# Kernel tuning notes

Measured on AMD Instinct MI355X. Metric: run time of the kernel, lower is better.

Reference implementation:

```python
import jax, jax.numpy as jnp
import numpy as np

N_NODES = 50000
N_EDGES = 800000
NODE_DIM = 8
EDGE_DIM = 4
ENC = 64
ROUNDS = 3
OUT_DIM = 5
NEG_SLOPE = 0.2


def _segment_softmax(s, dst, n):
    # per-destination-neighborhood softmax over edge scores s: [E]
    smax = jax.ops.segment_max(s, dst, num_segments=n)
    ex = jnp.exp(s - smax[dst])
    denom = jax.ops.segment_sum(ex, dst, num_segments=n)
    return ex / denom[dst]


def _gatv2(h, e_enc, src, dst, Wl, Wr, We, att, b):
    # GATv2Conv, heads=1, share_weights=False, no dropout (eval)
    xl = h @ Wl            # [N, ENC] source transform
    xr = h @ Wr            # [N, ENC] dest transform
    ep = e_enc @ We        # [E, ENC] edge transform
    m = xl[src] + xr[dst] + ep               # [E, ENC]
    s = jax.nn.leaky_relu(m, NEG_SLOPE) @ att  # [E]
    alpha = _segment_softmax(s, dst, h.shape[0])
    out = jax.ops.segment_sum(alpha[:, None] * xl[src], dst, num_segments=h.shape[0])
    return out + b


def _gnn_stack(h, e_enc, src, dst, Wl, Wr, We, att, b):
    for r in range(ROUNDS):
        h = _gatv2(h, e_enc, src, dst, Wl[r], Wr[r], We[r], att[r], b[r])
        if r < ROUNDS - 1:
            h = jax.nn.relu(h)
    return h


def setup_inputs() -> dict:
    key = jax.random.key(0)
    ks = jax.random.split(key, 24)
    f32 = jnp.float32
    p = lambda k, shp: 0.1 * jax.random.normal(k, shp, dtype=f32)
    return {
        "x": jax.random.normal(ks[0], (N_NODES, NODE_DIM), dtype=f32),
        "edge_attr": jax.random.normal(ks[1], (N_EDGES, EDGE_DIM), dtype=f32),
        "W_node": p(ks[2], (NODE_DIM, ENC)), "b_node": jnp.zeros((ENC,), f32),
        "W_edge": p(ks[3], (EDGE_DIM, ENC)), "b_edge": jnp.zeros((ENC,), f32),
        "actor_Wl": p(ks[4], (ROUNDS, ENC, ENC)),
        "actor_Wr": p(ks[5], (ROUNDS, ENC, ENC)),
        "actor_We": p(ks[6], (ROUNDS, ENC, ENC)),
        "actor_att": p(ks[7], (ROUNDS, ENC)),
        "actor_b": jnp.zeros((ROUNDS, ENC), f32),
        "critic_Wl": p(ks[8], (ROUNDS, ENC, ENC)),
        "critic_Wr": p(ks[9], (ROUNDS, ENC, ENC)),
        "critic_We": p(ks[10], (ROUNDS, ENC, ENC)),
        "critic_att": p(ks[11], (ROUNDS, ENC)),
        "critic_b": jnp.zeros((ROUNDS, ENC), f32),
        "W_act": p(ks[12], (ENC, OUT_DIM)), "b_act": jnp.zeros((OUT_DIM,), f32),
        "W_val": p(ks[13], (ENC, 1)), "b_val": jnp.zeros((1,), f32),
        "src": jax.random.randint(ks[14], (N_EDGES,), 0, N_NODES, dtype=jnp.int32),
        "dst": jax.random.randint(ks[15], (N_EDGES,), 0, N_NODES, dtype=jnp.int32),
    }


def reference(x, edge_attr, W_node, b_node, W_edge, b_edge,
              actor_Wl, actor_Wr, actor_We, actor_att, actor_b,
              critic_Wl, critic_Wr, critic_We, critic_att, critic_b,
              W_act, b_act, W_val, b_val, src, dst):
    h0 = x @ W_node + b_node          # node encoder (single SlimFC, no activation)
    e0 = edge_attr @ W_edge + b_edge  # edge encoder
    ha = _gnn_stack(h0, e0, src, dst, actor_Wl, actor_Wr, actor_We, actor_att, actor_b)
    hc = _gnn_stack(h0, e0, src, dst, critic_Wl, critic_Wr, critic_We, critic_att, critic_b)
    actions = jnp.tanh(ha @ W_act + b_act)  # action decoder, tanh activation
    values = hc @ W_val + b_val             # value decoder, no activation
    return jnp.concatenate([actions, values], axis=-1)  # [N, OUT_DIM+1]
```

## Files before the change

kernel.cpp:

```cpp
#include <hip/hip_runtime.h>
#include <math.h>

#define N_NODES 50000
#define N_EDGES 800000
#define ENC 64
#define ROUNDS 3
#define NEG_SLOPE 0.2f

typedef unsigned int u32;

__device__ __forceinline__ float lrelu(float m) {
  return m > 0.f ? m : NEG_SLOPE * m;
}

__global__ void k_hist(const int* __restrict__ dst, int* __restrict__ deg) {
  int i = blockIdx.x * blockDim.x + threadIdx.x;
  int stride = gridDim.x * blockDim.x;
  for (; i < N_EDGES; i += stride) atomicAdd(&deg[dst[i]], 1);
}

#define SCAN_BLOCKS ((N_NODES + 255) / 256)

__global__ void __launch_bounds__(256) k_red(const int* __restrict__ deg,
                                             int* __restrict__ part) {
  __shared__ int sm[256];
  int bi = blockIdx.x, t = threadIdx.x;
  int i = bi * 256 + t;
  sm[t] = (i < N_NODES) ? deg[i] : 0;
  __syncthreads();
  for (int off = 128; off > 0; off >>= 1) {
    if (t < off) sm[t] += sm[t + off];
    __syncthreads();
  }
  if (t == 0) part[bi] = sm[0];
}

__global__ void __launch_bounds__(256) k_scanp(int* __restrict__ part) {
  __shared__ int sm[256];
  int t = threadIdx.x;
  int v = (t < SCAN_BLOCKS) ? part[t] : 0;
  sm[t] = v;
  __syncthreads();
  for (int off = 1; off < 256; off <<= 1) {
    int u = (t >= off) ? sm[t - off] : 0;
    __syncthreads();
    sm[t] += u;
    __syncthreads();
  }
  if (t < SCAN_BLOCKS) part[t] = sm[t] - v;
}

__global__ void __launch_bounds__(256) k_csr(int* __restrict__ degcur,
                                             const int* __restrict__ part,
                                             int* __restrict__ row_start) {
  __shared__ int sm[256];
  int bi = blockIdx.x, t = threadIdx.x;
  int i = bi * 256 + t;
  int v = (i < N_NODES) ? degcur[i] : 0;
  sm[t] = v;
  __syncthreads();
  for (int off = 1; off < 256; off <<= 1) {
    int u = (t >= off) ? sm[t - off] : 0;
    __syncthreads();
    sm[t] += u;
    __syncthreads();
  }
  int excl = sm[t] - v + part[bi];
  if (i < N_NODES) {
    row_start[i] = excl;
    degcur[i] = excl;
    if (i == N_NODES - 1) row_start[N_NODES] = excl + v;
  }
}

__global__ void k_scatter(const int* __restrict__ src, const int* __restrict__ dst,
                          const float* __restrict__ ea, int* __restrict__ cursor,
                          int* __restrict__ srcs, float* __restrict__ ea_perm) {
  int i = blockIdx.x * blockDim.x + threadIdx.x;
  int stride = gridDim.x * blockDim.x;
  for (; i < N_EDGES; i += stride) {
    int d = dst[i];
    int pos = atomicAdd(&cursor[d], 1);
    srcs[pos] = src[i];
    ((float4*)ea_perm)[pos] = ((const float4*)ea)[i];
  }
}

__global__ void k_encode(const float* __restrict__ x, const float* __restrict__ Wn,
                         const float* __restrict__ bn, float* __restrict__ h0,
                         const float* __restrict__ W_edge, const float* __restrict__ b_edge,
                         const float* __restrict__ aWe, const float* __restrict__ cWe,
                         float* __restrict__ wcomb, float* __restrict__ bcomb) {
  __shared__ float lw[8 * ENC];
  __shared__ float lb[ENC];
  int t = threadIdx.x;
  if (blockIdx.x == 0) {
    int i = t >> 6, d = t & 63;
    for (int sr = 0; sr < 6; ++sr) {
      const float* We = (sr < 3) ? (aWe + sr * ENC * ENC) : (cWe + (sr - 3) * ENC * ENC);
      float sum = 0.f;
      for (int k = 0; k < ENC; ++k) sum += W_edge[i * ENC + k] * We[k * ENC + d];
      wcomb[sr * 4 * ENC + i * ENC + d] = sum;
      if (t < ENC) {
        float bs = 0.f;
        for (int k = 0; k < ENC; ++k) bs += b_edge[k] * We[k * ENC + t];
        bcomb[sr * ENC + t] = bs;
      }
    }
  }
  for (int i = t; i < 8 * ENC; i += blockDim.x) lw[i] = Wn[i];
  if (t < ENC) lb[t] = bn[t];
  __syncthreads();
  int wid = t >> 6, lane = t & 63;
  int nwaves = (blockDim.x >> 6) * gridDim.x;
  int w = blockIdx.x * (blockDim.x >> 6) + wid;
  for (int n = w; n < N_NODES; n += nwaves) {
    const float4* xr4 = (const float4*)(x + n * 8);
    float4 a = xr4[0], b = xr4[1];
    float acc = lb[lane];
    acc += a.x * lw[0 * ENC + lane] + a.y * lw[1 * ENC + lane] +
           a.z * lw[2 * ENC + lane] + a.w * lw[3 * ENC + lane];
    acc += b.x * lw[4 * ENC + lane] + b.y * lw[5 * ENC + lane] +
           b.z * lw[6 * ENC + lane] + b.w * lw[7 * ENC + lane];
    h0[n * ENC + lane] = acc;
  }
}

__global__ void __launch_bounds__(256) k_gemm2(const float* __restrict__ hinA,
                                               const float* __restrict__ hinC,
                                               const float* __restrict__ WlA,
                                               const float* __restrict__ WrA,
                                               const float* __restrict__ bcA,
                                               float* __restrict__ xlA_,
                                               float* __restrict__ xrA_,
                                               const float* __restrict__ WlC,
                                               const float* __restrict__ WrC,
                                               const float* __restrict__ bcC,
                                               float* __restrict__ xlC_,
                                               float* __restrict__ xrC_) {
  const int stk = blockIdx.y;
  const float* hin = stk ? hinC : hinA;
  const float* Wl = stk ? WlC : WlA;
  const float* Wr = stk ? WrC : WrA;
  const float* bc = stk ? bcC : bcA;
  float* xl = stk ? xlC_ : xlA_;
  float* xr = stk ? xrC_ : xrA_;
  __shared__ float lw[2 * ENC * ENC];
  __shared__ float lh[64 * ENC];
  int t = threadIdx.x;
  {
    const float4* wl4 = (const float4*)Wl;
    const float4* wr4 = (const float4*)Wr;
    float4* lw4 = (float4*)lw;
#pragma unroll
    for (int i = 0; i < 4; ++i) lw4[t + 256 * i] = wl4[t + 256 * i];
#pragma unroll
    for (int i = 0; i < 4; ++i) lw4[1024 + t + 256 * i] = wr4[t + 256 * i];
  }
  int base = blockIdx.x * 64;
  {
    const float4* h4 = (const float4*)hin;
    float4* lh4 = (float4*)lh;
    int maxi = N_NODES * 16 - 1;
#pragma unroll
    for (int i = 0; i < 4; ++i) {
      int idx = t + 256 * i;
      int gi = base * 16 + idx;
      if (gi > maxi) gi = maxi;
      lh4[idx] = h4[gi];
    }
  }
  __syncthreads();
  int wid = t >> 6, lane = t & 63;
  int msel = lane >> 5, cc = lane & 31;
  const float2* lw2 = (const float2*)lw;
  float* outp = msel ? xr : xl;
  float2 bcv = make_float2(0.f, 0.f);
  if (msel) bcv = ((const float2*)bc)[cc];
#pragma unroll
  for (int chunk = 0; chunk < 4; ++chunk) {
    int n0 = wid * 16 + chunk * 4;
    float a00 = 0.f, a01 = 0.f, a10 = 0.f, a11 = 0.f;
    float a20 = 0.f, a21 = 0.f, a30 = 0.f, a31 = 0.f;
    const float4* r0 = (const float4*)(lh + (n0 + 0) * ENC);
    const float4* r1 = (const float4*)(lh + (n0 + 1) * ENC);
    const float4* r2 = (const float4*)(lh + (n0 + 2) * ENC);
    const float4* r3 = (const float4*)(lh + (n0 + 3) * ENC);
#pragma unroll
    for (int k4 = 0; k4 < 16; ++k4) {
      float4 h0 = r0[k4], h1 = r1[k4], h2 = r2[k4], h3 = r3[k4];
      float2 w0 = lw2[msel * 2048 + (k4 * 4 + 0) * 32 + cc];
      float2 w1 = lw2[msel * 2048 + (k4 * 4 + 1) * 32 + cc];
      float2 w2 = lw2[msel * 2048 + (k4 * 4 + 2) * 32 + cc];
      float2 w3 = lw2[msel * 2048 + (k4 * 4 + 3) * 32 + cc];
      a00 += h0.x * w0.x + h0.y * w1.x + h0.z * w2.x + h0.w * w3.x;
      a01 += h0.x * w0.y + h0.y * w1.y + h0.z * w2.y + h0.w * w3.y;
      a10 += h1.x * w0.x + h1.y * w1.x + h1.z * w2.x + h1.w * w3.x;
      a11 += h1.x * w0.y + h1.y * w1.y + h1.z * w2.y + h1.w * w3.y;
      a20 += h2.x * w0.x + h2.y * w1.x + h2.z * w2.x + h2.w * w3.x;
      a21 += h2.x * w0.y + h2.y * w1.y + h2.z * w2.y + h2.w * w3.y;
      a30 += h3.x * w0.x + h3.y * w1.x + h3.z * w2.x + h3.w * w3.x;
      a31 += h3.x * w0.y + h3.y * w1.y + h3.z * w2.y + h3.w * w3.y;
    }
    int ng = base + n0;
    if (ng + 0 < N_NODES) *(float2*)(outp + (size_t)(ng + 0) * ENC + cc * 2) = make_float2(a00 + bcv.x, a01 + bcv.y);
    if (ng + 1 < N_NODES) *(float2*)(outp + (size_t)(ng + 1) * ENC + cc * 2) = make_float2(a10 + bcv.x, a11 + bcv.y);
    if (ng + 2 < N_NODES) *(float2*)(outp + (size_t)(ng + 2) * ENC + cc * 2) = make_float2(a20 + bcv.x, a21 + bcv.y);
    if (ng + 3 < N_NODES) *(float2*)(outp + (size_t)(ng + 3) * ENC + cc * 2) = make_float2(a30 + bcv.x, a31 + bcv.y);
  }
}

template <int RELU>
__global__ void __launch_bounds__(256) k_attn(
    const int* __restrict__ row_start, const int* __restrict__ srcs,
    const float* __restrict__ ea_perm,
    const float* __restrict__ xla, const float* __restrict__ xra,
    const float* __restrict__ xlc, const float* __restrict__ xrc,
    const float* __restrict__ wca, const float* __restrict__ wcc,
    const float* __restrict__ atta, const float* __restrict__ attc,
    const float* __restrict__ Ba, const float* __restrict__ Bc,
    float* __restrict__ ha, float* __restrict__ hc) {
  const float NEG_INF = __int_as_float(0xff800000u);
  const int stk = blockIdx.y;
  const float* xl = stk ? xlc : xla;
  const float* xr = stk ? xrc : xra;
  const float* wc = stk ? wcc : wca;
  const float* att = stk ? attc : atta;
  const float* B = stk ? Bc : Ba;
  float* hout = stk ? hc : ha;
  int t = threadIdx.x;
  int wid = t >> 6, lane = t & 63;
  int g = lane >> 4;
  int l16 = lane & 15;
  float4 w0 = ((const float4*)(wc + 0 * ENC))[l16];
  float4 w1 = ((const float4*)(wc + 1 * ENC))[l16];
  float4 w2 = ((const float4*)(wc + 2 * ENC))[l16];
  float4 w3 = ((const float4*)(wc + 3 * ENC))[l16];
  float4 at = ((const float4*)att)[l16];
  float4 bv = ((const float4*)B)[l16];
  int nw = (blockDim.x >> 6) * gridDim.x;
  for (int n = blockIdx.x * (blockDim.x >> 6) + wid; n < N_NODES; n += nw) {
    int rs = row_start[n], re = row_start[n + 1];
    float4 outv;
    if (re > rs) {
      float4 xrn = ((const float4*)(xr + (size_t)n * ENC))[l16];
      float m = -1e30f, den = 0.f;
      float4 acc = make_float4(0.f, 0.f, 0.f, 0.f);
      int cnt0 = re - rs; if (cnt0 > 16) cnt0 = 16;
      float eav = (lane < 4 * cnt0) ? ea_perm[(size_t)rs * 4 + lane] : 0.f;
      int sval = (lane < cnt0) ? srcs[rs + lane] : 0;
      for (int base = rs; base < re; base += 16) {
        int cnt = re - base; if (cnt > 16) cnt = 16;
        float eav_c = eav;
        int sval_c = sval;
        int nb = base + 16;
        if (nb < re) {
          int cn = re - nb; if (cn > 16) cn = 16;
          eav = (lane < 4 * cn) ? ea_perm[(size_t)nb * 4 + lane] : 0.f;
          sval = (lane < cn) ? srcs[nb + lane] : 0;
        }
        float4 la[4];
        bool act[4];
#pragma unroll
        for (int j = 0; j < 4; ++j) {
          int jj = j * 4 + g;
          act[j] = jj < cnt;
          int sj = __shfl(sval_c, act[j] ? jj : (cnt - 1));
          la[j] = ((const float4*)xl)[sj * 16 + l16];
        }
        float px[4];
#pragma unroll
        for (int j = 0; j < 4; ++j) {
          int jj = j * 4 + g;
          float av0 = __shfl(eav_c, jj * 4 + 0);
          float av1 = __shfl(eav_c, jj * 4 + 1);
          float av2 = __shfl(eav_c, jj * 4 + 2);
          float av3 = __shfl(eav_c, jj * 4 + 3);
          float p = lrelu(la[j].x + xrn.x + av0 * w0.x + av1 * w1.x + av2 * w2.x + av3 * w3.x) * at.x;
          p += lrelu(la[j].y + xrn.y + av0 * w0.y + av1 * w1.y + av2 * w2.y + av3 * w3.y) * at.y;
          p += lrelu(la[j].z + xrn.z + av0 * w0.z + av1 * w1.z + av2 * w2.z + av3 * w3.z) * at.z;
          p += lrelu(la[j].w + xrn.w + av0 * w0.w + av1 * w1.w + av2 * w2.w + av3 * w3.w) * at.w;
          p += __shfl_xor(p, 1);
          p += __shfl_xor(p, 2);
          p += __shfl_xor(p, 4);
          p += __shfl_xor(p, 8);
          px[j] = act[j] ? p : NEG_INF;
        }
#pragma unroll
        for (int j = 0; j < 4; ++j) {
          float mn = fmaxf(m, px[j]);
          float sc = __expf(m - mn);
          float ex = __expf(px[j] - mn);
          den = den * sc + ex;
          acc.x = acc.x * sc + ex * la[j].x;
          acc.y = acc.y * sc + ex * la[j].y;
          acc.z = acc.z * sc + ex * la[j].z;
          acc.w = acc.w * sc + ex * la[j].w;
          m = mn;
        }
      }
#pragma unroll
      for (int d = 16; d <= 32; d <<= 1) {
        float m2 = __shfl_xor(m, d);
        float dn2 = __shfl_xor(den, d);
        float a2x = __shfl_xor(acc.x, d), a2y = __shfl_xor(acc.y, d);
        float a2z = __shfl_xor(acc.z, d), a2w = __shfl_xor(acc.w, d);
        float mn = fmaxf(m, m2);
        float s1 = __expf(m - mn), s2 = __expf(m2 - mn);
        den = den * s1 + dn2 * s2;
        acc.x = acc.x * s1 + a2x * s2;
        acc.y = acc.y * s1 + a2y * s2;
        acc.z = acc.z * s1 + a2z * s2;
        acc.w = acc.w * s1 + a2w * s2;
        m = mn;
      }
      float inv = 1.f / den;
      outv = make_float4(acc.x * inv + bv.x, acc.y * inv + bv.y,
                         acc.z * inv + bv.z, acc.w * inv + bv.w);
    } else {
      outv = bv;
    }
    if (RELU) {
      outv.x = fmaxf(outv.x, 0.f);
      outv.y = fmaxf(outv.y, 0.f);
      outv.z = fmaxf(outv.z, 0.f);
      outv.w = fmaxf(outv.w, 0.f);
    }
    if (g == 0) ((float4*)(hout + (size_t)n * ENC))[l16] = outv;
  }
}

__global__ void k_dec(const float* __restrict__ ha, const float* __restrict__ hc,
                      const float* __restrict__ Wa, const float* __restrict__ ba,
                      const float* __restrict__ Wv, const float* __restrict__ bv,
                      float* __restrict__ out) {
  int t = threadIdx.x;
  int wid = t >> 6, lane = t & 63;
  int nw = (blockDim.x >> 6) * gridDim.x;
  int w = blockIdx.x * (blockDim.x >> 6) + wid;
  for (int n = w; n < N_NODES; n += nw) {
    float hva = ha[(size_t)n * ENC + lane];
    float hvc = hc[(size_t)n * ENC + lane];
#pragma unroll
    for (int j = 0; j < 5; ++j) {
      float p = hva * Wa[lane * 5 + j];
      p += __shfl_xor(p, 1);
      p += __shfl_xor(p, 2);
      p += __shfl_xor(p, 4);
      p += __shfl_xor(p, 8);
      p += __shfl_xor(p, 16);
      p += __shfl_xor(p, 32);
      if (lane == 0) out[n * 6 + j] = tanhf(p + ba[j]);
    }
    float p = hvc * Wv[lane];
    p += __shfl_xor(p, 1);
    p += __shfl_xor(p, 2);
    p += __shfl_xor(p, 4);
    p += __shfl_xor(p, 8);
    p += __shfl_xor(p, 16);
    p += __shfl_xor(p, 32);
    if (lane == 0) out[n * 6 + 5] = p + bv[0];
  }
}

extern "C" void kernel_launch(void* const* d_in, const int* in_sizes, int n_in,
                              void* d_out, int out_size, void* d_ws, size_t ws_size,
                              hipStream_t stream) {
  const float* x    = (const float*)d_in[0];
  const float* ea   = (const float*)d_in[1];
  const float* Wn   = (const float*)d_in[2];
  const float* bn   = (const float*)d_in[3];
  const float* Wedg = (const float*)d_in[4];
  const float* bedg = (const float*)d_in[5];
  const float* aWl  = (const float*)d_in[6];
  const float* aWr  = (const float*)d_in[7];
  const float* aWe  = (const float*)d_in[8];
  const float* aAtt = (const float*)d_in[9];
  const float* aB   = (const float*)d_in[10];
  const float* cWl  = (const float*)d_in[11];
  const float* cWr  = (const float*)d_in[12];
  const float* cWe  = (const float*)d_in[13];
  const float* cAtt = (const float*)d_in[14];
  const float* cB   = (const float*)d_in[15];
  const float* Wa   = (const float*)d_in[16];
  const float* ba   = (const float*)d_in[17];
  const float* Wv   = (const float*)d_in[18];
  const float* bv   = (const float*)d_in[19];
  const int* src    = (const int*)d_in[20];
  const int* dst    = (const int*)d_in[21];
  float* out = (float*)d_out;

  char* w = (char*)d_ws;
  size_t off = 0;
  auto alloc = [&](size_t bytes) -> char* {
    char* p = w + off;
    off = (off + bytes + 255) & ~(size_t)255;
    return p;
  };
  float* h0  = (float*)alloc((size_t)N_NODES * ENC * 4);
  float* hA  = (float*)alloc((size_t)N_NODES * ENC * 4);
  float* hC  = (float*)alloc((size_t)N_NODES * ENC * 4);
  float* xlA = (float*)alloc((size_t)N_NODES * ENC * 4);
  float* xrA = (float*)alloc((size_t)N_NODES * ENC * 4);
  float* xlC = (float*)alloc((size_t)N_NODES * ENC * 4);
  float* xrC = (float*)alloc((size_t)N_NODES * ENC * 4);
  int* srcs      = (int*)alloc((size_t)N_EDGES * 4);
  float* ea_perm = (float*)alloc((size_t)N_EDGES * 16);
  int* row_start = (int*)alloc((size_t)(N_NODES + 1) * 4);
  int* cursor    = (int*)alloc((size_t)N_NODES * 4);
  int* part      = (int*)alloc(256 * 4);
  float* wcomb   = (float*)alloc(6 * 4 * ENC * 4);
  float* bcomb   = (float*)alloc(6 * ENC * 4);

  hipMemsetAsync(cursor, 0, (size_t)N_NODES * 4, stream);
  k_hist<<<2048, 256, 0, stream>>>(dst, cursor);
  k_red<<<SCAN_BLOCKS, 256, 0, stream>>>(cursor, part);
  k_scanp<<<1, 256, 0, stream>>>(part);
  k_csr<<<SCAN_BLOCKS, 256, 0, stream>>>(cursor, part, row_start);
  k_scatter<<<2048, 256, 0, stream>>>(src, dst, ea, cursor, srcs, ea_perm);

  k_encode<<<512, 256, 0, stream>>>(x, Wn, bn, h0, Wedg, bedg, aWe, cWe, wcomb, bcomb);

  const int GEMM_TILES = (N_NODES + 63) / 64;

  for (int r = 0; r < ROUNDS; ++r) {
    const float* hinA = (r == 0) ? h0 : hA;
    const float* hinC = (r == 0) ? h0 : hC;
    k_gemm2<<<dim3(GEMM_TILES, 2), 256, 0, stream>>>(
        hinA, hinC, aWl + r * ENC * ENC, aWr + r * ENC * ENC, bcomb + r * ENC, xlA, xrA,
        cWl + r * ENC * ENC, cWr + r * ENC * ENC, bcomb + (3 + r) * ENC, xlC, xrC);
    if (r < ROUNDS - 1)
      k_attn<1><<<dim3(2048, 2), 256, 0, stream>>>(row_start, srcs, ea_perm, xlA, xrA, xlC, xrC,
                                                   wcomb + r * 4 * ENC, wcomb + (3 + r) * 4 * ENC,
                                                   aAtt + r * ENC, cAtt + r * ENC,
                                                   aB + r * ENC, cB + r * ENC, hA, hC);
    else
      k_attn<0><<<dim3(2048, 2), 256, 0, stream>>>(row_start, srcs, ea_perm, xlA, xrA, xlC, xrC,
                                                   wcomb + r * 4 * ENC, wcomb + (3 + r) * 4 * ENC,
                                                   aAtt + r * ENC, cAtt + r * ENC,
                                                   aB + r * ENC, cB + r * ENC, hA, hC);
  }
  k_dec<<<1024, 256, 0, stream>>>(hA, hC, Wa, ba, Wv, bv, out);
}
```

Baseline: 845.6 us.

## Interleave actor/critic xl/xr rows and process both stacks in one attention wave

The GEMM now writes actor and critic projections into combined arrays of 128 floats per node. The attention kernel handles both stacks in a single pass: each half-wave of 16 lanes serves one stack, and each 512-byte row gather fetches both stacks' features for an edge. This halves the number of passes over the CSR edge lists, source indices and edge attributes, and doubles the bytes per gathered row, so random-access efficiency should improve. In exchange, each wave now covers two edges per step instead of four, and the launch grid is halved, so per-node latency may rise.

Measured after the change: 689.8 us. 1.23x faster.

```diff
diff --git a/kernel.cpp b/kernel.cpp
--- a/kernel.cpp
+++ b/kernel.cpp
@@ -131,20 +131,16 @@
                                                const float* __restrict__ WlA,
                                                const float* __restrict__ WrA,
                                                const float* __restrict__ bcA,
-                                               float* __restrict__ xlA_,
-                                               float* __restrict__ xrA_,
                                                const float* __restrict__ WlC,
                                                const float* __restrict__ WrC,
                                                const float* __restrict__ bcC,
-                                               float* __restrict__ xlC_,
-                                               float* __restrict__ xrC_) {
+                                               float* __restrict__ xl_comb,
+                                               float* __restrict__ xr_comb) {
   const int stk = blockIdx.y;
   const float* hin = stk ? hinC : hinA;
   const float* Wl = stk ? WlC : WlA;
   const float* Wr = stk ? WrC : WrA;
   const float* bc = stk ? bcC : bcA;
-  float* xl = stk ? xlC_ : xlA_;
-  float* xr = stk ? xrC_ : xrA_;
   __shared__ float lw[2 * ENC * ENC];
   __shared__ float lh[64 * ENC];
   int t = threadIdx.x;
@@ -174,7 +170,7 @@
   int wid = t >> 6, lane = t & 63;
   int msel = lane >> 5, cc = lane & 31;
   const float2* lw2 = (const float2*)lw;
-  float* outp = msel ? xr : xl;
+  float* outp = (msel ? xr_comb : xl_comb) + stk * 64;
   float2 bcv = make_float2(0.f, 0.f);
   if (msel) bcv = ((const float2*)bc)[cc];
 #pragma unroll
@@ -203,10 +199,10 @@
       a31 += h3.x * w0.y + h3.y * w1.y + h3.z * w2.y + h3.w * w3.y;
     }
     int ng = base + n0;
-    if (ng + 0 < N_NODES) *(float2*)(outp + (size_t)(ng + 0) * ENC + cc * 2) = make_float2(a00 + bcv.x, a01 + bcv.y);
-    if (ng + 1 < N_NODES) *(float2*)(outp + (size_t)(ng + 1) * ENC + cc * 2) = make_float2(a10 + bcv.x, a11 + bcv.y);
-    if (ng + 2 < N_NODES) *(float2*)(outp + (size_t)(ng + 2) * ENC + cc * 2) = make_float2(a20 + bcv.x, a21 + bcv.y);
-    if (ng + 3 < N_NODES) *(float2*)(outp + (size_t)(ng + 3) * ENC + cc * 2) = make_float2(a30 + bcv.x, a31 + bcv.y);
+    if (ng + 0 < N_NODES) *(float2*)(outp + (size_t)(ng + 0) * 128 + cc * 2) = make_float2(a00 + bcv.x, a01 + bcv.y);
+    if (ng + 1 < N_NODES) *(float2*)(outp + (size_t)(ng + 1) * 128 + cc * 2) = make_float2(a10 + bcv.x, a11 + bcv.y);
+    if (ng + 2 < N_NODES) *(float2*)(outp + (size_t)(ng + 2) * 128 + cc * 2) = make_float2(a20 + bcv.x, a21 + bcv.y);
+    if (ng + 3 < N_NODES) *(float2*)(outp + (size_t)(ng + 3) * 128 + cc * 2) = make_float2(a30 + bcv.x, a31 + bcv.y);
   }
 }
 
@@ -214,36 +210,34 @@
 __global__ void __launch_bounds__(256) k_attn(
     const int* __restrict__ row_start, const int* __restrict__ srcs,
     const float* __restrict__ ea_perm,
-    const float* __restrict__ xla, const float* __restrict__ xra,
-    const float* __restrict__ xlc, const float* __restrict__ xrc,
+    const float* __restrict__ xl_comb, const float* __restrict__ xr_comb,
     const float* __restrict__ wca, const float* __restrict__ wcc,
     const float* __restrict__ atta, const float* __restrict__ attc,
     const float* __restrict__ Ba, const float* __restrict__ Bc,
     float* __restrict__ ha, float* __restrict__ hc) {
   const float NEG_INF = __int_as_float(0xff800000u);
-  const int stk = blockIdx.y;
-  const float* xl = stk ? xlc : xla;
-  const float* xr = stk ? xrc : xra;
-  const float* wc = stk ? wcc : wca;
-  const float* att = stk ? attc : atta;
-  const float* B = stk ? Bc : Ba;
-  float* hout = stk ? hc : ha;
   int t = threadIdx.x;
   int wid = t >> 6, lane = t & 63;
-  int g = lane >> 4;
+  int g2 = lane >> 5;
+  int sl = (lane >> 4) & 1;
   int l16 = lane & 15;
-  float4 w0 = ((const float4*)(wc + 0 * ENC))[l16];
-  float4 w1 = ((const float4*)(wc + 1 * ENC))[l16];
-  float4 w2 = ((const float4*)(wc + 2 * ENC))[l16];
-  float4 w3 = ((const float4*)(wc + 3 * ENC))[l16];
-  float4 at = ((const float4*)att)[l16];
-  float4 bv = ((const float4*)B)[l16];
+  int q32 = lane & 31;
+  const float* wcS = sl ? wcc : wca;
+  const float* attS = sl ? attc : atta;
+  const float* BS = sl ? Bc : Ba;
+  float* houtS = sl ? hc : ha;
+  float4 w0 = ((const float4*)(wcS + 0 * ENC))[l16];
+  float4 w1 = ((const float4*)(wcS + 1 * ENC))[l16];
+  float4 w2 = ((const float4*)(wcS + 2 * ENC))[l16];
+  float4 w3 = ((const float4*)(wcS + 3 * ENC))[l16];
+  float4 at = ((const float4*)attS)[l16];
+  float4 bv = ((const float4*)BS)[l16];
   int nw = (blockDim.x >> 6) * gridDim.x;
   for (int n = blockIdx.x * (blockDim.x >> 6) + wid; n < N_NODES; n += nw) {
     int rs = row_start[n], re = row_start[n + 1];
     float4 outv;
     if (re > rs) {
-      float4 xrn = ((const float4*)(xr + (size_t)n * ENC))[l16];
+      float4 xrn = ((const float4*)xr_comb)[(size_t)n * 32 + q32];
       float m = -1e30f, den = 0.f;
       float4 acc = make_float4(0.f, 0.f, 0.f, 0.f);
       int cnt0 = re - rs; if (cnt0 > 16) cnt0 = 16;
@@ -259,52 +253,66 @@
           eav = (lane < 4 * cn) ? ea_perm[(size_t)nb * 4 + lane] : 0.f;
           sval = (lane < cn) ? srcs[nb + lane] : 0;
         }
-        float4 la[4];
-        bool act[4];
-#pragma unroll
-        for (int j = 0; j < 4; ++j) {
-          int jj = j * 4 + g;
-          act[j] = jj < cnt;
-          int sj = __shfl(sval_c, act[j] ? jj : (cnt - 1));
-          la[j] = ((const float4*)xl)[sj * 16 + l16];
-        }
-        float px[4];
-#pragma unroll
-        for (int j = 0; j < 4; ++j) {
-          int jj = j * 4 + g;
-          float av0 = __shfl(eav_c, jj * 4 + 0);
-          float av1 = __shfl(eav_c, jj * 4 + 1);
-          float av2 = __shfl(eav_c, jj * 4 + 2);
-          float av3 = __shfl(eav_c, jj * 4 + 3);
-          float p = lrelu(la[j].x + xrn.x + av0 * w0.x + av1 * w1.x + av2 * w2.x + av3 * w3.x) * at.x;
-          p += lrelu(la[j].y + xrn.y + av0 * w0.y + av1 * w1.y + av2 * w2.y + av3 * w3.y) * at.y;
-          p += lrelu(la[j].z + xrn.z + av0 * w0.z + av1 * w1.z + av2 * w2.z + av3 * w3.z) * at.z;
-          p += lrelu(la[j].w + xrn.w + av0 * w0.w + av1 * w1.w + av2 * w2.w + av3 * w3.w) * at.w;
-          p += __shfl_xor(p, 1);
-          p += __shfl_xor(p, 2);
-          p += __shfl_xor(p, 4);
-          p += __shfl_xor(p, 8);
-          px[j] = act[j] ? p : NEG_INF;
-        }
-#pragma unroll
-        for (int j = 0; j < 4; ++j) {
-          float mn = fmaxf(m, px[j]);
-          float sc = __expf(m - mn);
-          float ex = __expf(px[j] - mn);
-          den = den * sc + ex;
-          acc.x = acc.x * sc + ex * la[j].x;
-          acc.y = acc.y * sc + ex * la[j].y;
-          acc.z = acc.z * sc + ex * la[j].z;
-          acc.w = acc.w * sc + ex * la[j].w;
-          m = mn;
+        for (int jp = 0; jp < 4; ++jp) {
+          if (jp * 4 >= cnt) break;
+          int jjA = jp * 4 + g2;
+          int jjB = jjA + 2;
+          bool actA = jjA < cnt, actB = jjB < cnt;
+          int snA = __shfl(sval_c, actA ? jjA : 0);
+          int snB = __shfl(sval_c, actB ? jjB : 0);
+          float4 laA = ((const float4*)xl_comb)[(size_t)snA * 32 + q32];
+          float4 laB = ((const float4*)xl_comb)[(size_t)snB * 32 + q32];
+          float aA0 = __shfl(eav_c, jjA * 4 + 0);
+          float aA1 = __shfl(eav_c, jjA * 4 + 1);
+          float aA2 = __shfl(eav_c, jjA * 4 + 2);
+          float aA3 = __shfl(eav_c, jjA * 4 + 3);
+          float aB0 = __shfl(eav_c, jjB * 4 + 0);
+          float aB1 = __shfl(eav_c, jjB * 4 + 1);
+          float aB2 = __shfl(eav_c, jjB * 4 + 2);
+          float aB3 = __shfl(eav_c, jjB * 4 + 3);
+          float pA = lrelu(laA.x + xrn.x + aA0 * w0.x + aA1 * w1.x + aA2 * w2.x + aA3 * w3.x) * at.x;
+          pA += lrelu(laA.y + xrn.y + aA0 * w0.y + aA1 * w1.y + aA2 * w2.y + aA3 * w3.y) * at.y;
+          pA += lrelu(laA.z + xrn.z + aA0 * w0.z + aA1 * w1.z + aA2 * w2.z + aA3 * w3.z) * at.z;
+          pA += lrelu(laA.w + xrn.w + aA0 * w0.w + aA1 * w1.w + aA2 * w2.w + aA3 * w3.w) * at.w;
+          float pB = lrelu(laB.x + xrn.x + aB0 * w0.x + aB1 * w1.x + aB2 * w2.x + aB3 * w3.x) * at.x;
+          pB += lrelu(laB.y + xrn.y + aB0 * w0.y + aB1 * w1.y + aB2 * w2.y + aB3 * w3.y) * at.y;
+          pB += lrelu(laB.z + xrn.z + aB0 * w0.z + aB1 * w1.z + aB2 * w2.z + aB3 * w3.z) * at.z;
+          pB += lrelu(laB.w + xrn.w + aB0 * w0.w + aB1 * w1.w + aB2 * w2.w + aB3 * w3.w) * at.w;
+          pA += __shfl_xor(pA, 1); pB += __shfl_xor(pB, 1);
+          pA += __shfl_xor(pA, 2); pB += __shfl_xor(pB, 2);
+          pA += __shfl_xor(pA, 4); pB += __shfl_xor(pB, 4);
+          pA += __shfl_xor(pA, 8); pB += __shfl_xor(pB, 8);
+          pA = actA ? pA : NEG_INF;
+          pB = actB ? pB : NEG_INF;
+          {
+            float mn = fmaxf(m, pA);
+            float sc = __expf(m - mn);
+            float ex = __expf(pA - mn);
+            den = den * sc + ex;
+            acc.x = acc.x * sc + ex * laA.x;
+            acc.y = acc.y * sc + ex * laA.y;
+            acc.z = acc.z * sc + ex * laA.z;
+            acc.w = acc.w * sc + ex * laA.w;
+            m = mn;
+          }
+          {
+            float mn = fmaxf(m, pB);
+            float sc = __expf(m - mn);
+            float ex = __expf(pB - mn);
+            den = den * sc + ex;
+            acc.x = acc.x * sc + ex * laB.x;
+            acc.y = acc.y * sc + ex * laB.y;
+            acc.z = acc.z * sc + ex * laB.z;
+            acc.w = acc.w * sc + ex * laB.w;
+            m = mn;
+          }
         }
       }
-#pragma unroll
-      for (int d = 16; d <= 32; d <<= 1) {
-        float m2 = __shfl_xor(m, d);
-        float dn2 = __shfl_xor(den, d);
-        float a2x = __shfl_xor(acc.x, d), a2y = __shfl_xor(acc.y, d);
-        float a2z = __shfl_xor(acc.z, d), a2w = __shfl_xor(acc.w, d);
+      {
+        float m2 = __shfl_xor(m, 32);
+        float dn2 = __shfl_xor(den, 32);
+        float a2x = __shfl_xor(acc.x, 32), a2y = __shfl_xor(acc.y, 32);
+        float a2z = __shfl_xor(acc.z, 32), a2w = __shfl_xor(acc.w, 32);
         float mn = fmaxf(m, m2);
         float s1 = __expf(m - mn), s2 = __expf(m2 - mn);
         den = den * s1 + dn2 * s2;
@@ -312,7 +320,6 @@
         acc.y = acc.y * s1 + a2y * s2;
         acc.z = acc.z * s1 + a2z * s2;
         acc.w = acc.w * s1 + a2w * s2;
-        m = mn;
       }
       float inv = 1.f / den;
       outv = make_float4(acc.x * inv + bv.x, acc.y * inv + bv.y,
@@ -326,7 +333,7 @@
       outv.z = fmaxf(outv.z, 0.f);
       outv.w = fmaxf(outv.w, 0.f);
     }
-    if (g == 0) ((float4*)(hout + (size_t)n * ENC))[l16] = outv;
+    if (g2 == 0) ((float4*)houtS)[(size_t)n * 16 + l16] = outv;
   }
 }
 
@@ -400,10 +407,8 @@
   float* h0  = (float*)alloc((size_t)N_NODES * ENC * 4);
   float* hA  = (float*)alloc((size_t)N_NODES * ENC * 4);
   float* hC  = (float*)alloc((size_t)N_NODES * ENC * 4);
-  float* xlA = (float*)alloc((size_t)N_NODES * ENC * 4);
-  float* xrA = (float*)alloc((size_t)N_NODES * ENC * 4);
-  float* xlC = (float*)alloc((size_t)N_NODES * ENC * 4);
-  float* xrC = (float*)alloc((size_t)N_NODES * ENC * 4);
+  float* xl_comb = (float*)alloc((size_t)N_NODES * 2 * ENC * 4);
+  float* xr_comb = (float*)alloc((size_t)N_NODES * 2 * ENC * 4);
   int* srcs      = (int*)alloc((size_t)N_EDGES * 4);
   float* ea_perm = (float*)alloc((size_t)N_EDGES * 16);
   int* row_start = (int*)alloc((size_t)(N_NODES + 1) * 4);
@@ -427,18 +432,19 @@
     const float* hinA = (r == 0) ? h0 : hA;
     const float* hinC = (r == 0) ? h0 : hC;
     k_gemm2<<<dim3(GEMM_TILES, 2), 256, 0, stream>>>(
-        hinA, hinC, aWl + r * ENC * ENC, aWr + r * ENC * ENC, bcomb + r * ENC, xlA, xrA,
-        cWl + r * ENC * ENC, cWr + r * ENC * ENC, bcomb + (3 + r) * ENC, xlC, xrC);
+        hinA, hinC, aWl + r * ENC * ENC, aWr + r * ENC * ENC, bcomb + r * ENC,
+        cWl + r * ENC * ENC, cWr + r * ENC * ENC, bcomb + (3 + r) * ENC,
+        xl_comb, xr_comb);
     if (r < ROUNDS - 1)
-      k_attn<1><<<dim3(2048, 2), 256, 0, stream>>>(row_start, srcs, ea_perm, xlA, xrA, xlC, xrC,
-                                                   wcomb + r * 4 * ENC, wcomb + (3 + r) * 4 * ENC,
-                                                   aAtt + r * ENC, cAtt + r * ENC,
-                                                   aB + r * ENC, cB + r * ENC, hA, hC);
+      k_attn<1><<<2048, 256, 0, stream>>>(row_start, srcs, ea_perm, xl_comb, xr_comb,
+                                          wcomb + r * 4 * ENC, wcomb + (3 + r) * 4 * ENC,
+                                          aAtt + r * ENC, cAtt + r * ENC,
+                                          aB + r * ENC, cB + r * ENC, hA, hC);
     else
-      k_attn<0><<<dim3(2048, 2), 256, 0, stream>>>(row_start, srcs, ea_perm, xlA, xrA, xlC, xrC,
-                                                   wcomb + r * 4 * ENC, wcomb + (3 + r) * 4 * ENC,
-                                                   aAtt + r * ENC, cAtt + r * ENC,
-                                                   aB + r * ENC, cB + r * ENC, hA, hC);
+      k_attn<0><<<2048, 256, 0, stream>>>(row_start, srcs, ea_perm, xl_comb, xr_comb,
+                                          wcomb + r * 4 * ENC, wcomb + (3 + r) * 4 * ENC,
+                                          aAtt + r * ENC, cAtt + r * ENC,
+                                          aB + r * ENC, cB + r * ENC, hA, hC);
   }
   k_dec<<<1024, 256, 0, stream>>>(hA, hC, Wa, ba, Wv, bv, out);
 }
```
